# Kernel tuning notes

Measured on AMD Instinct MI355X. Metric: run time of the kernel, lower is better.

## Reference

```python
import jax, jax.numpy as jnp
import numpy as np

D = 1024
H = 16
DH = D // H
SCALE = DH ** -0.5
EPS = 1e-5


def setup_inputs() -> dict:
    key = jax.random.key(0)
    ks = jax.random.split(key, 8)
    B, K = 256, 64
    hidden = jax.random.normal(ks[0], (B, K, D), dtype=jnp.float32)
    active_mask = jax.random.bernoulli(ks[1], 0.5, (B, K))
    w = lambda k: jax.random.normal(k, (D, D), dtype=jnp.float32) * 0.02
    return {
        "hidden": hidden,
        "active_mask": active_mask,
        "W_q": w(ks[2]),
        "W_k": w(ks[3]),
        "W_v": w(ks[4]),
        "W_o": w(ks[5]),
        "ln_gamma": jnp.ones((D,), dtype=jnp.float32),
        "ln_beta": jnp.zeros((D,), dtype=jnp.float32),
    }


def reference(hidden, active_mask, W_q, W_k, W_v, W_o, ln_gamma, ln_beta):
    B, K, _ = hidden.shape
    # Linear (no bias): x @ W.T, then split heads -> [B, H, K, Dh]
    def heads(t):
        return t.reshape(B, K, H, DH).transpose(0, 2, 1, 3)
    Q = heads(hidden @ W_q.T)
    Km = heads(hidden @ W_k.T)
    V = heads(hidden @ W_v.T)
    # scaled dot-product scores [B, H, K, K]
    attn = jnp.einsum("bhqd,bhkd->bhqk", Q, Km) * SCALE
    attn = jax.nn.softmax(attn, axis=-1)
    # post-softmax row masking: inactive query rows get zero attention
    row_mask = active_mask[:, None, :, None].astype(attn.dtype)  # [B,1,K,1]
    attn = attn * row_mask
    out = jnp.einsum("bhqk,bhkd->bhqd", attn, V)
    out = out.transpose(0, 2, 1, 3).reshape(B, K, D)
    out = out @ W_o.T
    # gated residual: residual attention output only on active modules
    active_f = active_mask[:, :, None].astype(hidden.dtype)
    h_final = hidden + active_f * out
    # LayerNorm over last dim
    mu = jnp.mean(h_final, axis=-1, keepdims=True)
    var = jnp.var(h_final, axis=-1, keepdims=True)
    h_norm = (h_final - mu) * jax.lax.rsqrt(var + EPS)
    return h_norm * ln_gamma + ln_beta
```

## Files before the change

kernel.cpp:

```cpp
#include <hip/hip_runtime.h>
#include <hip/hip_bf16.h>
#include <stdint.h>

#define D_DIM 1024
#define NH 16
#define DHD 64
#define SEQ 64
#define NBATCH 256
#define M_TOT 16384
#define ATT_SCALE 0.125f
#define LN_EPS 1e-5f

typedef __attribute__((ext_vector_type(8))) short bf16x8;
typedef __attribute__((ext_vector_type(4))) float f32x4;

__device__ __forceinline__ float bf2f(short s) {
  union { uint32_t u; float f; } c;
  c.u = ((uint32_t)(uint16_t)s) << 16;
  return c.f;
}

__device__ __forceinline__ short f2bf(float f) {
  union { __hip_bfloat16 h; short s; } c; c.h = __float2bfloat16(f);
  return c.s;
}

__device__ __forceinline__ bf16x8 cvt8(float4 a, float4 b) {
  bf16x8 r;
  r[0] = f2bf(a.x); r[1] = f2bf(a.y); r[2] = f2bf(a.z); r[3] = f2bf(a.w);
  r[4] = f2bf(b.x); r[5] = f2bf(b.y); r[6] = f2bf(b.z); r[7] = f2bf(b.w);
  return r;
}

__device__ __forceinline__ void cp16(const void* g, void* l) {
  __builtin_amdgcn_global_load_lds(
      (const __attribute__((address_space(1))) uint32_t*)g,
      (__attribute__((address_space(3))) uint32_t*)l, 16, 0, 0);
}

__global__ void conv_all(const float* __restrict__ Wq, const float* __restrict__ Wk,
                         const float* __restrict__ Wv, const float* __restrict__ Wo,
                         const float* __restrict__ H,
                         __hip_bfloat16* __restrict__ Wall,
                         __hip_bfloat16* __restrict__ Hb) {
  const size_t idx8 = ((size_t)blockIdx.x * 256 + threadIdx.x) * 8;
  const size_t WE = (size_t)4 * D_DIM * D_DIM;
  const float* src;
  __hip_bfloat16* dst;
  if (idx8 < WE) {
    int z = (int)(idx8 >> 20);
    size_t off = idx8 & ((1u << 20) - 1);
    src = ((z == 0) ? Wq : (z == 1) ? Wk : (z == 2) ? Wv : Wo) + off;
    dst = Wall + idx8;
  } else {
    size_t off = idx8 - WE;
    src = H + off;
    dst = Hb + off;
  }
  float4 a = ((const float4*)src)[0];
  float4 b = ((const float4*)src)[1];
  *(bf16x8*)(short*)dst = cvt8(a, b);
}

__global__ void gemm_qkv_bf(const __hip_bfloat16* __restrict__ Hb,
                            const __hip_bfloat16* __restrict__ Wall,
                            __hip_bfloat16* __restrict__ Qw,
                            __hip_bfloat16* __restrict__ Kw,
                            __hip_bfloat16* __restrict__ Vtw) {
  __shared__ __align__(16) __hip_bfloat16 As[128 * 32];
  __shared__ __align__(16) __hip_bfloat16 Bs[128 * 32];
  const int tid = threadIdx.x;
  const int lane = tid & 63;
  const int wave = tid >> 6;
  const int l16 = lane & 15, kq = lane >> 4;
  const int m0 = blockIdx.x * 128, n0 = blockIdx.y * 128;
  const int z = blockIdx.z;
  const __hip_bfloat16* Bm = Wall + (size_t)z * D_DIM * D_DIM;
  const int wr = (wave >> 1) * 64, wc = (wave & 1) * 64;

  f32x4 acc[4][4] = {};

  for (int kk = 0; kk < D_DIM; kk += 32) {
#pragma unroll
    for (int i = 0; i < 2; ++i) {
      int chunk = i * 256 + tid;
      int r = chunk >> 2, c8 = (chunk & 3) << 3;
      int ldsb = (i * 256 + wave * 64) * 16;
      cp16(Hb + (size_t)(m0 + r) * D_DIM + kk + c8, (char*)As + ldsb);
      cp16(Bm + (size_t)(n0 + r) * D_DIM + kk + c8, (char*)Bs + ldsb);
    }
    __syncthreads();
    bf16x8 af[4], bfr[4];
#pragma unroll
    for (int i = 0; i < 4; ++i)
      af[i] = *(const bf16x8*)((const short*)As + (wr + i * 16 + l16) * 32 + kq * 8);
#pragma unroll
    for (int j = 0; j < 4; ++j)
      bfr[j] = *(const bf16x8*)((const short*)Bs + (wc + j * 16 + l16) * 32 + kq * 8);
#pragma unroll
    for (int i = 0; i < 4; ++i)
#pragma unroll
      for (int j = 0; j < 4; ++j)
        acc[i][j] = __builtin_amdgcn_mfma_f32_16x16x32_bf16(af[i], bfr[j], acc[i][j], 0, 0, 0);
    __syncthreads();
  }

  __hip_bfloat16* outp = (z == 0) ? Qw : (z == 1) ? Kw : Vtw;
#pragma unroll
  for (int i = 0; i < 4; ++i) {
#pragma unroll
    for (int r = 0; r < 4; ++r) {
      int gm = m0 + wr + i * 16 + kq * 4 + r;
      int b = gm >> 6, ks = gm & 63;
#pragma unroll
      for (int j = 0; j < 4; ++j) {
        int gn = n0 + wc + j * 16 + l16;
        int h = gn >> 6, dh = gn & 63;
        size_t idx = (z < 2)
            ? ((size_t)(b * NH + h) * SEQ + ks) * DHD + dh
            : ((size_t)(b * NH + h) * DHD + dh) * SEQ + ks;
        outp[idx] = __float2bfloat16(acc[i][j][r]);
      }
    }
  }
}

__global__ void attn_v2(__hip_bfloat16* Qw,
                        const __hip_bfloat16* __restrict__ Kw,
                        const __hip_bfloat16* __restrict__ Vtw,
                        const int* __restrict__ mask) {
  __shared__ __align__(16) __hip_bfloat16 Ps[4][16 * 72];
  const int tid = threadIdx.x;
  const int lane = tid & 63;
  const int wave = tid >> 6;
  const int l16 = lane & 15, kq = lane >> 4;
  const int hh = blockIdx.x * 4 + wave;
  const int b = hh >> 4;
  const size_t base = (size_t)hh * 4096;
  __hip_bfloat16* Pw = &Ps[wave][0];

  bf16x8 kf[2][4], vf[2][4], qf[4][2];
#pragma unroll
  for (int kk2 = 0; kk2 < 2; ++kk2)
#pragma unroll
    for (int j = 0; j < 4; ++j) {
      kf[kk2][j] = *(const bf16x8*)(Kw + base + (j * 16 + l16) * 64 + kk2 * 32 + kq * 8);
      vf[kk2][j] = *(const bf16x8*)(Vtw + base + (j * 16 + l16) * 64 + kk2 * 32 + kq * 8);
    }
#pragma unroll
  for (int qt = 0; qt < 4; ++qt)
#pragma unroll
    for (int kk2 = 0; kk2 < 2; ++kk2)
      qf[qt][kk2] = *(const bf16x8*)(Qw + base + (qt * 16 + l16) * 64 + kk2 * 32 + kq * 8);

#pragma unroll
  for (int qt = 0; qt < 4; ++qt) {
    f32x4 accS[4] = {};
#pragma unroll
    for (int kk2 = 0; kk2 < 2; ++kk2)
#pragma unroll
      for (int j = 0; j < 4; ++j)
        accS[j] = __builtin_amdgcn_mfma_f32_16x16x32_bf16(qf[qt][kk2], kf[kk2][j],
                                                          accS[j], 0, 0, 0);
#pragma unroll
    for (int r = 0; r < 4; ++r) {
      float sv[4];
      float m = -1e30f;
#pragma unroll
      for (int j = 0; j < 4; ++j) { sv[j] = accS[j][r] * ATT_SCALE; m = fmaxf(m, sv[j]); }
#pragma unroll
      for (int off = 1; off < 16; off <<= 1) m = fmaxf(m, __shfl_xor(m, off, 64));
      float s = 0.f;
#pragma unroll
      for (int j = 0; j < 4; ++j) { sv[j] = __expf(sv[j] - m); s += sv[j]; }
#pragma unroll
      for (int off = 1; off < 16; off <<= 1) s += __shfl_xor(s, off, 64);
      float inv = 1.0f / s;
      int ql = kq * 4 + r;
#pragma unroll
      for (int j = 0; j < 4; ++j)
        Pw[ql * 72 + j * 16 + l16] = __float2bfloat16(sv[j] * inv);
    }
    __asm volatile("s_waitcnt lgkmcnt(0)" ::: "memory");

    f32x4 accO[4] = {};
#pragma unroll
    for (int kk2 = 0; kk2 < 2; ++kk2) {
      bf16x8 a = *(const bf16x8*)((const short*)Pw + l16 * 72 + kk2 * 32 + kq * 8);
#pragma unroll
      for (int j = 0; j < 4; ++j)
        accO[j] = __builtin_amdgcn_mfma_f32_16x16x32_bf16(a, vf[kk2][j], accO[j], 0, 0, 0);
    }
    __asm volatile("s_waitcnt lgkmcnt(0)" ::: "memory");

#pragma unroll
    for (int r = 0; r < 4; ++r) {
      int q = qt * 16 + kq * 4 + r;
      float mk = mask[b * SEQ + q] ? 1.0f : 0.0f;
#pragma unroll
      for (int j = 0; j < 4; ++j)
        Qw[base + q * DHD + j * 16 + l16] = __float2bfloat16(accO[j][r] * mk);
    }
  }
}

__global__ void gemm_o(const __hip_bfloat16* __restrict__ Ow,
                       const __hip_bfloat16* __restrict__ WoB,
                       const int* __restrict__ mask,
                       __hip_bfloat16* Hb) {
  __shared__ __align__(16) __hip_bfloat16 As[128 * 32];
  __shared__ __align__(16) __hip_bfloat16 Bs[128 * 32];
  const int tid = threadIdx.x;
  const int lane = tid & 63;
  const int wave = tid >> 6;
  const int l16 = lane & 15, kq = lane >> 4;
  const int m0 = blockIdx.x * 128, n0 = blockIdx.y * 128;
  const int wr = (wave >> 1) * 64, wc = (wave & 1) * 64;

  f32x4 acc[4][4] = {};

  for (int kk = 0; kk < D_DIM; kk += 32) {
#pragma unroll
    for (int i = 0; i < 2; ++i) {
      int chunk = i * 256 + tid;
      int r = chunk >> 2, c8 = (chunk & 3) << 3;
      int ldsb = (i * 256 + wave * 64) * 16;
      int t = m0 + r, f = kk + c8;
      int b = t >> 6, s = t & 63, h = f >> 6, dh = f & 63;
      cp16(Ow + ((size_t)((b << 4) + h) << 12) + (s << 6) + dh, (char*)As + ldsb);
      cp16(WoB + (size_t)(n0 + r) * D_DIM + kk + c8, (char*)Bs + ldsb);
    }
    __syncthreads();
    bf16x8 af[4], bfr[4];
#pragma unroll
    for (int i = 0; i < 4; ++i)
      af[i] = *(const bf16x8*)((const short*)As + (wr + i * 16 + l16) * 32 + kq * 8);
#pragma unroll
    for (int j = 0; j < 4; ++j)
      bfr[j] = *(const bf16x8*)((const short*)Bs + (wc + j * 16 + l16) * 32 + kq * 8);
#pragma unroll
    for (int i = 0; i < 4; ++i)
#pragma unroll
      for (int j = 0; j < 4; ++j)
        acc[i][j] = __builtin_amdgcn_mfma_f32_16x16x32_bf16(af[i], bfr[j], acc[i][j], 0, 0, 0);
    __syncthreads();
  }

#pragma unroll
  for (int i = 0; i < 4; ++i) {
#pragma unroll
    for (int r = 0; r < 4; ++r) {
      int gm = m0 + wr + i * 16 + kq * 4 + r;
      float mk = mask[gm] ? 1.0f : 0.0f;
#pragma unroll
      for (int j = 0; j < 4; ++j) {
        int gn = n0 + wc + j * 16 + l16;
        size_t idx = (size_t)gm * D_DIM + gn;
        Hb[idx] = __float2bfloat16(__bfloat162float(Hb[idx]) + mk * acc[i][j][r]);
      }
    }
  }
}

__global__ void ln_bf(const __hip_bfloat16* __restrict__ Hf,
                      const float* __restrict__ gamma,
                      const float* __restrict__ beta,
                      float* __restrict__ out) {
  __shared__ float red[4];
  const int row = blockIdx.x, tid = threadIdx.x;
  const int wave = tid >> 6, lane = tid & 63;
  const size_t boff = (size_t)row * D_DIM + tid * 8;

  bf16x8 v = *(const bf16x8*)((const short*)Hf + boff);
  float f[8], s = 0.f, ss = 0.f;
#pragma unroll
  for (int k = 0; k < 8; ++k) { f[k] = bf2f(v[k]); s += f[k]; ss += f[k] * f[k]; }
#pragma unroll
  for (int off = 1; off < 64; off <<= 1) {
    s += __shfl_xor(s, off, 64);
    ss += __shfl_xor(ss, off, 64);
  }
  if (lane == 0) { red[wave * 2] = s; red[wave * 2 + 1] = ss; }
  __syncthreads();
  s = red[0] + red[2];
  ss = red[1] + red[3];
  const float mu = s * (1.0f / D_DIM);
  const float var = ss * (1.0f / D_DIM) - mu * mu;
  const float rs = rsqrtf(var + LN_EPS);

  float4 g0 = ((const float4*)(gamma + tid * 8))[0];
  float4 g1 = ((const float4*)(gamma + tid * 8))[1];
  float4 b0 = ((const float4*)(beta + tid * 8))[0];
  float4 b1 = ((const float4*)(beta + tid * 8))[1];
  float g[8] = {g0.x, g0.y, g0.z, g0.w, g1.x, g1.y, g1.z, g1.w};
  float bb[8] = {b0.x, b0.y, b0.z, b0.w, b1.x, b1.y, b1.z, b1.w};
  float o[8];
#pragma unroll
  for (int k = 0; k < 8; ++k)
    o[k] = (f[k] - mu) * rs * g[k] + bb[k];
  ((float4*)(out + boff))[0] = make_float4(o[0], o[1], o[2], o[3]);
  ((float4*)(out + boff))[1] = make_float4(o[4], o[5], o[6], o[7]);
}

extern "C" void kernel_launch(void* const* d_in, const int* in_sizes, int n_in,
                              void* d_out, int out_size, void* d_ws, size_t ws_size,
                              hipStream_t stream) {
  const float* hidden = (const float*)d_in[0];
  const int* mask = (const int*)d_in[1];
  const float* Wq = (const float*)d_in[2];
  const float* Wk = (const float*)d_in[3];
  const float* Wv = (const float*)d_in[4];
  const float* Wo = (const float*)d_in[5];
  const float* gamma = (const float*)d_in[6];
  const float* beta = (const float*)d_in[7];
  float* out = (float*)d_out;

  const size_t SZ = (size_t)M_TOT * D_DIM;
  __hip_bfloat16* Hb   = (__hip_bfloat16*)d_ws;
  __hip_bfloat16* Kw   = Hb + SZ;
  __hip_bfloat16* Qw   = Hb + 2 * SZ;
  __hip_bfloat16* Vtw  = Hb + 3 * SZ;
  __hip_bfloat16* Wall = Hb + 4 * SZ;

  conv_all<<<dim3(10240), 256, 0, stream>>>(Wq, Wk, Wv, Wo, hidden, Wall, Hb);
  gemm_qkv_bf<<<dim3(128, 8, 3), 256, 0, stream>>>(Hb, Wall, Qw, Kw, Vtw);
  attn_v2<<<dim3(1024), 256, 0, stream>>>(Qw, Kw, Vtw, mask);
  gemm_o<<<dim3(128, 8), 256, 0, stream>>>(Qw, Wall + 3 * D_DIM * D_DIM, mask, Hb);
  ln_bf<<<dim3(16384), 128, 0, stream>>>(Hb, gamma, beta, out);
}
```

Baseline: 365.6 us.

## Rewrite QKV and O GEMMs with 256x256 tiles and double-buffered pipelined LDS

Both projection GEMMs move from 128x128 tiles with single-buffered LDS to 256x256 tiles, BK=64 and 512 threads. The LDS layout is XOR-swizzled to avoid bank conflicts. The k-loop is software-pipelined: the next tile's async copies are interleaved with MFMA phases, using barriers, setprio and vmcnt waits. The goal is to hide global-load latency and raise MFMA utilisation and data reuse, at the cost of more registers and LDS (128KB per block) and fewer blocks (768 for QKV, 256 for O).

```diff
diff --git a/kernel.cpp b/kernel.cpp
--- a/kernel.cpp
+++ b/kernel.cpp
@@ -10,6 +10,11 @@
 #define M_TOT 16384
 #define ATT_SCALE 0.125f
 #define LN_EPS 1e-5f
+
+#define BM 256
+#define BN 256
+#define BKT 64
+#define NTK (D_DIM / BKT)
 
 typedef __attribute__((ext_vector_type(8))) short bf16x8;
 typedef __attribute__((ext_vector_type(4))) float f32x4;
@@ -62,64 +67,158 @@
   *(bf16x8*)(short*)dst = cvt8(a, b);
 }
 
-__global__ void gemm_qkv_bf(const __hip_bfloat16* __restrict__ Hb,
-                            const __hip_bfloat16* __restrict__ Wall,
-                            __hip_bfloat16* __restrict__ Qw,
-                            __hip_bfloat16* __restrict__ Kw,
-                            __hip_bfloat16* __restrict__ Vtw) {
-  __shared__ __align__(16) __hip_bfloat16 As[128 * 32];
-  __shared__ __align__(16) __hip_bfloat16 Bs[128 * 32];
+#define GEMM_TILE(J, CUR, NXT) do {                                           \
+    const int jn_ = (J) + 1;                                                  \
+          \
+    _Pragma("unroll") for (int i_ = 0; i_ < 4; ++i_) {                        \
+      af[i_][0] = *(const bf16x8*)(LdsA[CUR] + aoff + i_ * 2048 + colsw0);    \
+      af[i_][1] = *(const bf16x8*)(LdsA[CUR] + aoff + i_ * 2048 + colsw1);    \
+    }                                                                         \
+    _Pragma("unroll") for (int q_ = 0; q_ < 2; ++q_) {                        \
+      bfr[q_][0] = *(const bf16x8*)(LdsB[CUR] + boff + q_ * 2048 + colsw0);   \
+      bfr[q_][1] = *(const bf16x8*)(LdsB[CUR] + boff + q_ * 2048 + colsw1);   \
+    }                                                                         \
+    if (jn_ < NTK) { STG_A(NXT, jn_, 2); STG_A(NXT, jn_, 3); }                \
+    __builtin_amdgcn_s_barrier();                                             \
+    __asm volatile("s_waitcnt lgkmcnt(0)" ::: "memory");                      \
+    __builtin_amdgcn_s_setprio(1);                                            \
+    _Pragma("unroll") for (int i_ = 0; i_ < 4; ++i_)                          \
+      _Pragma("unroll") for (int q_ = 0; q_ < 2; ++q_) {                      \
+        acc[i_][q_] = __builtin_amdgcn_mfma_f32_16x16x32_bf16(                \
+            af[i_][0], bfr[q_][0], acc[i_][q_], 0, 0, 0);                     \
+        acc[i_][q_] = __builtin_amdgcn_mfma_f32_16x16x32_bf16(                \
+            af[i_][1], bfr[q_][1], acc[i_][q_], 0, 0, 0);                     \
+      }                                                                       \
+    __builtin_amdgcn_s_setprio(0);                                            \
+    __builtin_amdgcn_s_barrier();                                             \
+                        \
+    _Pragma("unroll") for (int q_ = 0; q_ < 2; ++q_) {                        \
+      bfr[2 + q_][0] =                                                        \
+          *(const bf16x8*)(LdsB[CUR] + boff + (2 + q_) * 2048 + colsw0);      \
+      bfr[2 + q_][1] =                                                        \
+          *(const bf16x8*)(LdsB[CUR] + boff + (2 + q_) * 2048 + colsw1);      \
+    }                                                                         \
+    if (jn_ < NTK) { STG_B(NXT, jn_, 0); STG_B(NXT, jn_, 1); }                \
+    __builtin_amdgcn_s_barrier();                                             \
+    __asm volatile("s_waitcnt lgkmcnt(0)" ::: "memory");                      \
+    __builtin_amdgcn_s_setprio(1);                                            \
+    _Pragma("unroll") for (int i_ = 0; i_ < 4; ++i_)                          \
+      _Pragma("unroll") for (int q_ = 0; q_ < 2; ++q_) {                      \
+        acc[i_][2 + q_] = __builtin_amdgcn_mfma_f32_16x16x32_bf16(            \
+            af[i_][0], bfr[2 + q_][0], acc[i_][2 + q_], 0, 0, 0);             \
+        acc[i_][2 + q_] = __builtin_amdgcn_mfma_f32_16x16x32_bf16(            \
+            af[i_][1], bfr[2 + q_][1], acc[i_][2 + q_], 0, 0, 0);             \
+      }                                                                       \
+    __builtin_amdgcn_s_setprio(0);                                            \
+    __builtin_amdgcn_s_barrier();                                             \
+         \
+    _Pragma("unroll") for (int i_ = 0; i_ < 4; ++i_) {                        \
+      af[i_][0] =                                                             \
+          *(const bf16x8*)(LdsA[CUR] + aoff + 8192 + i_ * 2048 + colsw0);     \
+      af[i_][1] =                                                             \
+          *(const bf16x8*)(LdsA[CUR] + aoff + 8192 + i_ * 2048 + colsw1);     \
+    }                                                                         \
+    if (jn_ < NTK) { STG_B(NXT, jn_, 2); STG_B(NXT, jn_, 3); }                \
+    __builtin_amdgcn_s_barrier();                                             \
+    __asm volatile("s_waitcnt lgkmcnt(0)" ::: "memory");                      \
+    __builtin_amdgcn_s_setprio(1);                                            \
+    _Pragma("unroll") for (int i_ = 0; i_ < 4; ++i_)                          \
+      _Pragma("unroll") for (int q_ = 0; q_ < 2; ++q_) {                      \
+        acc[4 + i_][2 + q_] = __builtin_amdgcn_mfma_f32_16x16x32_bf16(        \
+            af[i_][0], bfr[2 + q_][0], acc[4 + i_][2 + q_], 0, 0, 0);         \
+        acc[4 + i_][2 + q_] = __builtin_amdgcn_mfma_f32_16x16x32_bf16(        \
+            af[i_][1], bfr[2 + q_][1], acc[4 + i_][2 + q_], 0, 0, 0);         \
+      }                                                                       \
+    __builtin_amdgcn_s_setprio(0);                                            \
+    __builtin_amdgcn_s_barrier();                                             \
+    \
+     \
+    if ((J) + 2 < NTK) { STG_A(CUR, (J) + 2, 0); STG_A(CUR, (J) + 2, 1); }    \
+    __builtin_amdgcn_s_barrier();                                             \
+    __builtin_amdgcn_s_setprio(1);                                            \
+    _Pragma("unroll") for (int i_ = 0; i_ < 4; ++i_)                          \
+      _Pragma("unroll") for (int q_ = 0; q_ < 2; ++q_) {                      \
+        acc[4 + i_][q_] = __builtin_amdgcn_mfma_f32_16x16x32_bf16(            \
+            af[i_][0], bfr[q_][0], acc[4 + i_][q_], 0, 0, 0);                 \
+        acc[4 + i_][q_] = __builtin_amdgcn_mfma_f32_16x16x32_bf16(            \
+            af[i_][1], bfr[q_][1], acc[4 + i_][q_], 0, 0, 0);                 \
+      }                                                                       \
+    __builtin_amdgcn_s_setprio(0);                                            \
+    if ((J) + 2 < NTK) {                                                      \
+      __asm volatile("s_waitcnt vmcnt(2)" ::: "memory");                      \
+    } else if (jn_ < NTK) {                                                   \
+      __asm volatile("s_waitcnt vmcnt(0)" ::: "memory");                      \
+    }                                                                         \
+    __builtin_amdgcn_s_barrier();                                             \
+  } while (0)
+
+#define GEMM_PIPELINE() do {                                                  \
+            \
+    STG_A(0, 0, 0); STG_A(0, 0, 1); STG_A(0, 0, 2); STG_A(0, 0, 3);           \
+    STG_B(0, 0, 0); STG_B(0, 0, 1); STG_B(0, 0, 2); STG_B(0, 0, 3);           \
+    STG_A(1, 1, 0); STG_A(1, 1, 1);                                           \
+    __asm volatile("s_waitcnt vmcnt(2)" ::: "memory");                        \
+    __builtin_amdgcn_s_barrier();                                             \
+    _Pragma("unroll 1") for (int it_ = 0; it_ < NTK / 2; ++it_) {             \
+      GEMM_TILE(2 * it_, 0, 1);                                               \
+      GEMM_TILE(2 * it_ + 1, 1, 0);                                           \
+    }                                                                         \
+  } while (0)
+
+__global__ void __launch_bounds__(512, 2)
+gemm_qkv_bf(const __hip_bfloat16* __restrict__ Hb,
+            const __hip_bfloat16* __restrict__ Wall,
+            __hip_bfloat16* __restrict__ Qw,
+            __hip_bfloat16* __restrict__ Kw,
+            __hip_bfloat16* __restrict__ Vtw) {
+  __shared__ __align__(16) char LdsA[2][BM * BKT * 2];
+  __shared__ __align__(16) char LdsB[2][BN * BKT * 2];
   const int tid = threadIdx.x;
-  const int lane = tid & 63;
-  const int wave = tid >> 6;
+  const int lane = tid & 63, wave = tid >> 6;
   const int l16 = lane & 15, kq = lane >> 4;
-  const int m0 = blockIdx.x * 128, n0 = blockIdx.y * 128;
-  const int z = blockIdx.z;
-  const __hip_bfloat16* Bm = Wall + (size_t)z * D_DIM * D_DIM;
-  const int wr = (wave >> 1) * 64, wc = (wave & 1) * 64;
-
-  f32x4 acc[4][4] = {};
-
-  for (int kk = 0; kk < D_DIM; kk += 32) {
-#pragma unroll
-    for (int i = 0; i < 2; ++i) {
-      int chunk = i * 256 + tid;
-      int r = chunk >> 2, c8 = (chunk & 3) << 3;
-      int ldsb = (i * 256 + wave * 64) * 16;
-      cp16(Hb + (size_t)(m0 + r) * D_DIM + kk + c8, (char*)As + ldsb);
-      cp16(Bm + (size_t)(n0 + r) * D_DIM + kk + c8, (char*)Bs + ldsb);
-    }
-    __syncthreads();
-    bf16x8 af[4], bfr[4];
-#pragma unroll
-    for (int i = 0; i < 4; ++i)
-      af[i] = *(const bf16x8*)((const short*)As + (wr + i * 16 + l16) * 32 + kq * 8);
-#pragma unroll
-    for (int j = 0; j < 4; ++j)
-      bfr[j] = *(const bf16x8*)((const short*)Bs + (wc + j * 16 + l16) * 32 + kq * 8);
-#pragma unroll
-    for (int i = 0; i < 4; ++i)
-#pragma unroll
-      for (int j = 0; j < 4; ++j)
-        acc[i][j] = __builtin_amdgcn_mfma_f32_16x16x32_bf16(af[i], bfr[j], acc[i][j], 0, 0, 0);
-    __syncthreads();
-  }
-
-  __hip_bfloat16* outp = (z == 0) ? Qw : (z == 1) ? Kw : Vtw;
-#pragma unroll
-  for (int i = 0; i < 4; ++i) {
+  const int wr = wave >> 2, wc = wave & 3;
+  const int m0 = blockIdx.x * BM, n0 = blockIdx.y * BN;
+  const __hip_bfloat16* Bm = Wall + (size_t)blockIdx.z * D_DIM * D_DIM;
+  const int wub = wave * 1024;
+  const int srow = tid >> 3;
+  const int scol8 = (((tid >> 3) & 7) ^ (tid & 7)) << 3;
+  const size_t a_thr = (size_t)(m0 + srow) * D_DIM + scol8;
+  const size_t b_thr = (size_t)(n0 + srow) * D_DIM + scol8;
+  const int colsw0 = (kq * 16) ^ ((l16 & 7) << 4);
+  const int colsw1 = (64 + kq * 16) ^ ((l16 & 7) << 4);
+  const int aoff = (wr * 128 + l16) * 128;
+  const int boff = (wc * 64 + l16) * 128;
+
+  f32x4 acc[8][4] = {};
+  bf16x8 af[4][2], bfr[4][2];
+
+#define STG_A(BUF, JT, Q)                                                      \
+  cp16(Hb + a_thr + (size_t)(Q) * (64 * D_DIM) + (JT) * BKT,                   \
+       LdsA[BUF] + (Q) * 8192 + wub)
+#define STG_B(BUF, JT, Q)                                                      \
+  cp16(Bm + b_thr + (size_t)(Q) * (64 * D_DIM) + (JT) * BKT,                   \
+       LdsB[BUF] + (Q) * 8192 + wub)
+
+  GEMM_PIPELINE();
+
+#undef STG_A
+#undef STG_B
+
+  __hip_bfloat16* outp = (blockIdx.z == 0) ? Qw : (blockIdx.z == 1) ? Kw : Vtw;
+  const int zlt2 = (blockIdx.z < 2);
+#pragma unroll
+  for (int i = 0; i < 8; ++i) {
 #pragma unroll
     for (int r = 0; r < 4; ++r) {
-      int gm = m0 + wr + i * 16 + kq * 4 + r;
+      int gm = m0 + wr * 128 + i * 16 + kq * 4 + r;
       int b = gm >> 6, ks = gm & 63;
 #pragma unroll
-      for (int j = 0; j < 4; ++j) {
-        int gn = n0 + wc + j * 16 + l16;
+      for (int jf = 0; jf < 4; ++jf) {
+        int gn = n0 + wc * 64 + jf * 16 + l16;
         int h = gn >> 6, dh = gn & 63;
-        size_t idx = (z < 2)
-            ? ((size_t)(b * NH + h) * SEQ + ks) * DHD + dh
-            : ((size_t)(b * NH + h) * DHD + dh) * SEQ + ks;
-        outp[idx] = __float2bfloat16(acc[i][j][r]);
+        size_t idx = zlt2 ? ((size_t)(b * NH + h) * SEQ + ks) * DHD + dh
+                          : ((size_t)(b * NH + h) * DHD + dh) * SEQ + ks;
+        outp[idx] = __float2bfloat16(acc[i][jf][r]);
       }
     }
   }
@@ -204,59 +303,54 @@
   }
 }
 
-__global__ void gemm_o(const __hip_bfloat16* __restrict__ Ow,
-                       const __hip_bfloat16* __restrict__ WoB,
-                       const int* __restrict__ mask,
-                       __hip_bfloat16* Hb) {
-  __shared__ __align__(16) __hip_bfloat16 As[128 * 32];
-  __shared__ __align__(16) __hip_bfloat16 Bs[128 * 32];
+__global__ void __launch_bounds__(512, 2)
+gemm_o(const __hip_bfloat16* __restrict__ Ow,
+       const __hip_bfloat16* __restrict__ WoB,
+       const int* __restrict__ mask,
+       __hip_bfloat16* Hb) {
+  __shared__ __align__(16) char LdsA[2][BM * BKT * 2];
+  __shared__ __align__(16) char LdsB[2][BN * BKT * 2];
   const int tid = threadIdx.x;
-  const int lane = tid & 63;
-  const int wave = tid >> 6;
+  const int lane = tid & 63, wave = tid >> 6;
   const int l16 = lane & 15, kq = lane >> 4;
-  const int m0 = blockIdx.x * 128, n0 = blockIdx.y * 128;
-  const int wr = (wave >> 1) * 64, wc = (wave & 1) * 64;
-
-  f32x4 acc[4][4] = {};
-
-  for (int kk = 0; kk < D_DIM; kk += 32) {
-#pragma unroll
-    for (int i = 0; i < 2; ++i) {
-      int chunk = i * 256 + tid;
-      int r = chunk >> 2, c8 = (chunk & 3) << 3;
-      int ldsb = (i * 256 + wave * 64) * 16;
-      int t = m0 + r, f = kk + c8;
-      int b = t >> 6, s = t & 63, h = f >> 6, dh = f & 63;
-      cp16(Ow + ((size_t)((b << 4) + h) << 12) + (s << 6) + dh, (char*)As + ldsb);
-      cp16(WoB + (size_t)(n0 + r) * D_DIM + kk + c8, (char*)Bs + ldsb);
-    }
-    __syncthreads();
-    bf16x8 af[4], bfr[4];
-#pragma unroll
-    for (int i = 0; i < 4; ++i)
-      af[i] = *(const bf16x8*)((const short*)As + (wr + i * 16 + l16) * 32 + kq * 8);
-#pragma unroll
-    for (int j = 0; j < 4; ++j)
-      bfr[j] = *(const bf16x8*)((const short*)Bs + (wc + j * 16 + l16) * 32 + kq * 8);
-#pragma unroll
-    for (int i = 0; i < 4; ++i)
-#pragma unroll
-      for (int j = 0; j < 4; ++j)
-        acc[i][j] = __builtin_amdgcn_mfma_f32_16x16x32_bf16(af[i], bfr[j], acc[i][j], 0, 0, 0);
-    __syncthreads();
-  }
-
-#pragma unroll
-  for (int i = 0; i < 4; ++i) {
+  const int wr = wave >> 2, wc = wave & 3;
+  const int m0 = blockIdx.x * BM, n0 = blockIdx.y * BN;
+  const int wub = wave * 1024;
+  const int srow = tid >> 3;
+  const int scol8 = (((tid >> 3) & 7) ^ (tid & 7)) << 3;
+  const size_t ao_thr = ((size_t)(m0 >> 6) << 16) + (srow << 6) + scol8;
+  const size_t b_thr = (size_t)(n0 + srow) * D_DIM + scol8;
+  const int colsw0 = (kq * 16) ^ ((l16 & 7) << 4);
+  const int colsw1 = (64 + kq * 16) ^ ((l16 & 7) << 4);
+  const int aoff = (wr * 128 + l16) * 128;
+  const int boff = (wc * 64 + l16) * 128;
+
+  f32x4 acc[8][4] = {};
+  bf16x8 af[4][2], bfr[4][2];
+
+#define STG_A(BUF, JT, Q)                                                      \
+  cp16(Ow + ao_thr + ((size_t)(Q) << 16) + ((size_t)(JT) << 12),               \
+       LdsA[BUF] + (Q) * 8192 + wub)
+#define STG_B(BUF, JT, Q)                                                      \
+  cp16(WoB + b_thr + (size_t)(Q) * (64 * D_DIM) + (JT) * BKT,                  \
+       LdsB[BUF] + (Q) * 8192 + wub)
+
+  GEMM_PIPELINE();
+
+#undef STG_A
+#undef STG_B
+
+#pragma unroll
+  for (int i = 0; i < 8; ++i) {
 #pragma unroll
     for (int r = 0; r < 4; ++r) {
-      int gm = m0 + wr + i * 16 + kq * 4 + r;
+      int gm = m0 + wr * 128 + i * 16 + kq * 4 + r;
       float mk = mask[gm] ? 1.0f : 0.0f;
 #pragma unroll
-      for (int j = 0; j < 4; ++j) {
-        int gn = n0 + wc + j * 16 + l16;
+      for (int jf = 0; jf < 4; ++jf) {
+        int gn = n0 + wc * 64 + jf * 16 + l16;
         size_t idx = (size_t)gm * D_DIM + gn;
-        Hb[idx] = __float2bfloat16(__bfloat162float(Hb[idx]) + mk * acc[i][j][r]);
+        Hb[idx] = __float2bfloat16(__bfloat162float(Hb[idx]) + mk * acc[i][jf][r]);
       }
     }
   }
@@ -323,8 +417,8 @@
   __hip_bfloat16* Wall = Hb + 4 * SZ;
 
   conv_all<<<dim3(10240), 256, 0, stream>>>(Wq, Wk, Wv, Wo, hidden, Wall, Hb);
-  gemm_qkv_bf<<<dim3(128, 8, 3), 256, 0, stream>>>(Hb, Wall, Qw, Kw, Vtw);
+  gemm_qkv_bf<<<dim3(64, 4, 3), 512, 0, stream>>>(Hb, Wall, Qw, Kw, Vtw);
   attn_v2<<<dim3(1024), 256, 0, stream>>>(Qw, Kw, Vtw, mask);
-  gemm_o<<<dim3(128, 8), 256, 0, stream>>>(Qw, Wall + 3 * D_DIM * D_DIM, mask, Hb);
+  gemm_o<<<dim3(64, 4), 512, 0, stream>>>(Qw, Wall + 3 * D_DIM * D_DIM, mask, Hb);
   ln_bf<<<dim3(16384), 128, 0, stream>>>(Hb, gamma, beta, out);
 }
```

New measurement: 340.7 us. 6.8% less time.
